# Performance work log

Hardware: AMD Instinct MI355X
Metric: run time of the kernel (lower is better)

## Reference

```python
import jax, jax.numpy as jnp
import numpy as np

D = 1024
H = 16
DH = D // H
F = 4096
B, S = 4, 2048
EPS = 1e-5


def _ln(x, g, b):
    m = jnp.mean(x, axis=-1, keepdims=True)
    v = jnp.var(x, axis=-1, keepdims=True)
    return (x - m) * jax.lax.rsqrt(v + EPS) * g + b


def setup_inputs() -> dict:
    key = jax.random.key(0)
    ks = jax.random.split(key, 16)
    s = 0.02
    return {
        "x": jax.random.normal(ks[0], (B, S, D), jnp.float32),
        "key_padding_mask": jnp.zeros((B, S), jnp.bool_),
        "Wq": jax.random.normal(ks[1], (D, D), jnp.float32) * s,
        "bq": jnp.zeros((D,), jnp.float32),
        "Wk": jax.random.normal(ks[2], (D, D), jnp.float32) * s,
        "bk": jnp.zeros((D,), jnp.float32),
        "Wv": jax.random.normal(ks[3], (D, D), jnp.float32) * s,
        "bv": jnp.zeros((D,), jnp.float32),
        "Wo": jax.random.normal(ks[4], (D, D), jnp.float32) * s,
        "bo": jnp.zeros((D,), jnp.float32),
        "W1": jax.random.normal(ks[5], (F, D), jnp.float32) * s,
        "b1": jnp.zeros((F,), jnp.float32),
        "W2": jax.random.normal(ks[6], (D, F), jnp.float32) * s,
        "b2": jnp.zeros((D,), jnp.float32),
        "ln1_g": jnp.ones((D,), jnp.float32),
        "ln1_b": jnp.zeros((D,), jnp.float32),
        "ln2_g": jnp.ones((D,), jnp.float32),
        "ln2_b": jnp.zeros((D,), jnp.float32),
    }


def _attn(x, kpm, Wq, bq, Wk, bk, Wv, bv, Wo, bo):
    b, s, d = x.shape
    scaling = DH ** (-0.5)
    q = (x @ Wq.T + bq) * scaling
    k = x @ Wk.T + bk
    v = x @ Wv.T + bv
    q = q.reshape(b, s, H, DH)
    k = k.reshape(b, s, H, DH)
    v = v.reshape(b, s, H, DH)
    # [b,h,q,k]
    scores = jnp.einsum("bqhd,bkhd->bhqk", q, k)
    scores = jnp.where(kpm[:, None, None, :], -jnp.inf, scores)
    p = jax.nn.softmax(scores.astype(jnp.float32), axis=-1).astype(q.dtype)
    out = jnp.einsum("bhqk,bkhd->bqhd", p, v).reshape(b, s, d)
    return out @ Wo.T + bo


def reference(x, key_padding_mask, Wq, bq, Wk, bk, Wv, bv, Wo, bo,
              W1, b1, W2, b2, ln1_g, ln1_b, ln2_g, ln2_b):
    # post-LN (normalize_before=False), dropout in eval mode (identity)
    x = _ln(x + _attn(x, key_padding_mask, Wq, bq, Wk, bk, Wv, bv, Wo, bo), ln1_g, ln1_b)
    h = jax.nn.gelu(x @ W1.T + b1, approximate=False)
    x = _ln(x + (h @ W2.T + b2), ln2_g, ln2_b)
    return x
```

## Files before the change

kernel.cpp:

```cpp
#include <hip/hip_runtime.h>
#include <hip/hip_bf16.h>
#include <math.h>

typedef short bf16x8 __attribute__((ext_vector_type(8)));
typedef float f32x4 __attribute__((ext_vector_type(4)));

__device__ __forceinline__ unsigned short f2bfu(float f) {
    __hip_bfloat16 h = __float2bfloat16(f);
    return __builtin_bit_cast(unsigned short, h);
}

__device__ __forceinline__ float fexp2(float x) {
    float r;
    asm("v_exp_f32 %0, %1" : "=v"(r) : "v"(x));
    return r;
}

__device__ __forceinline__ unsigned cvtpk_bf16(float lo, float hi) {
    unsigned r;
    asm("v_cvt_pk_bf16_f32 %0, %1, %2" : "=v"(r) : "v"(lo), "v"(hi));
    return r;
}

__device__ __forceinline__ float gelu_fast(float x) {
    const float x2 = x * x;
    const float z = x * (0.7978845608f + 0.0356774081f * x2);
    const float e = fexp2(z * 2.88539008f);
    const float r = __builtin_amdgcn_rcpf(e + 1.0f);
    return x * (1.0f - r);
}

__device__ __forceinline__ void gload_lds16(const void* gsrc, void* ldst) {
    __builtin_amdgcn_global_load_lds((const __attribute__((address_space(1))) void*)gsrc,
                                     (__attribute__((address_space(3))) void*)ldst,
                                     16, 0, 0);
}

__global__ __launch_bounds__(256)
void cvt_bf16_kernel(const float4* __restrict__ in, ushort4* __restrict__ out, int n4) {
    int i = blockIdx.x * 256 + threadIdx.x;
    if (i >= n4) return;
    float4 v = in[i];
    ushort4 o;
    o.x = f2bfu(v.x); o.y = f2bfu(v.y); o.z = f2bfu(v.z); o.w = f2bfu(v.w);
    out[i] = o;
}

enum { EPI_QKV = 0, EPI_RESF32 = 2, EPI_GELU = 3, EPI_RESBF16 = 5 };

template<int EPI>
__global__ __launch_bounds__(256, 3)
void gemm_bt(const __hip_bfloat16* __restrict__ A,
             const __hip_bfloat16* __restrict__ W,
             const float* __restrict__ bias,
             const void* __restrict__ resv,
             float scale,
             void* __restrict__ outp, void* __restrict__ outp2, void* __restrict__ outp3,
             int M, int N, int K)
{
    __shared__ __hip_bfloat16 As[3][128 * 32];
    __shared__ __hip_bfloat16 Ws[3][128 * 32];
    const int tid = threadIdx.x;
    const int lane = tid & 63;
    const int wid = tid >> 6;
    const int wr = wid >> 1, wc = wid & 1;
    const int g = lane >> 4, lr = lane & 15;
    const int row0 = blockIdx.x * 128;
    const int col0 = blockIdx.y * 128;

    f32x4 acc[4][4];
    const f32x4 zero = {0.f, 0.f, 0.f, 0.f};
#pragma unroll
    for (int m = 0; m < 4; ++m)
#pragma unroll
        for (int n = 0; n < 4; ++n) acc[m][n] = zero;

    const int c0 = tid, c1 = tid + 256;
    const int ar0 = c0 >> 2, ac0 = (c0 & 3) * 8;
    const int ar1 = c1 >> 2, ac1 = (c1 & 3) * 8;
    const __hip_bfloat16* Arow0 = A + (size_t)(row0 + ar0) * K + ac0;
    const __hip_bfloat16* Arow1 = A + (size_t)(row0 + ar1) * K + ac1;
    const __hip_bfloat16* Wrow0 = W + (size_t)(col0 + ar0) * K + ac0;
    const __hip_bfloat16* Wrow1 = W + (size_t)(col0 + ar1) * K + ac1;

    auto stage = [&](int bi, int k0) {
        gload_lds16(Arow0 + k0, (char*)As[bi] + c0 * 16);
        gload_lds16(Arow1 + k0, (char*)As[bi] + c1 * 16);
        gload_lds16(Wrow0 + k0, (char*)Ws[bi] + c0 * 16);
        gload_lds16(Wrow1 + k0, (char*)Ws[bi] + c1 * 16);
    };

    const int NT = K >> 5;
    stage(0, 0);
    stage(1, 32);
    asm volatile("s_waitcnt vmcnt(4)" ::: "memory");
    __builtin_amdgcn_s_barrier();
    __builtin_amdgcn_sched_barrier(0);

    int cur = 0, stg = 2;
    int kpre = 64;
    for (int t = 0; t < NT; ++t) {
        if (t + 2 < NT) stage(stg, kpre);

        bf16x8 af[4], wf[4];
#pragma unroll
        for (int m = 0; m < 4; ++m)
            af[m] = *(const bf16x8*)(As[cur] + (wr * 64 + m * 16 + lr) * 32 + g * 8);
#pragma unroll
        for (int n = 0; n < 4; ++n)
            wf[n] = *(const bf16x8*)(Ws[cur] + (wc * 64 + n * 16 + lr) * 32 + g * 8);
#pragma unroll
        for (int m = 0; m < 4; ++m)
#pragma unroll
            for (int n = 0; n < 4; ++n)
                acc[m][n] = __builtin_amdgcn_mfma_f32_16x16x32_bf16(af[m], wf[n], acc[m][n], 0, 0, 0);

        if (t + 1 < NT) {
            if (t + 2 < NT) asm volatile("s_waitcnt vmcnt(4)" ::: "memory");
            else            asm volatile("s_waitcnt vmcnt(0)" ::: "memory");
            __builtin_amdgcn_s_barrier();
            __builtin_amdgcn_sched_barrier(0);
        }
        cur = (cur == 2) ? 0 : cur + 1;
        stg = (stg == 2) ? 0 : stg + 1;
        kpre += 32;
    }

#pragma unroll
    for (int n = 0; n < 4; ++n) {
        const int cc = col0 + wc * 64 + n * 16 + lr;
        const float bv = bias[cc];
#pragma unroll
        for (int m = 0; m < 4; ++m) {
            const int rbase = row0 + wr * 64 + m * 16 + g * 4;
            if (EPI == EPI_QKV) {
                const int seg = col0 >> 10;
                if (seg == 2) {
                    ushort4 u;
                    u.x = f2bfu(acc[m][n][0] + bv);
                    u.y = f2bfu(acc[m][n][1] + bv);
                    u.z = f2bfu(acc[m][n][2] + bv);
                    u.w = f2bfu(acc[m][n][3] + bv);
                    const int cc2 = cc - 2048;
                    const int h_ = cc2 >> 6, dh = cc2 & 63;
                    const int bb = rbase >> 11;
                    const int s = rbase & 2047;
                    *(ushort4*)((__hip_bfloat16*)outp3 +
                                (((size_t)bb * 16 + h_) * 64 + dh) * 2048 + s) = u;
                } else {
                    const float sc = (seg == 0) ? scale : 1.0f;
                    __hip_bfloat16* dst = (seg == 0) ? (__hip_bfloat16*)outp
                                                     : (__hip_bfloat16*)outp2;
                    const int ccl = cc & 1023;
#pragma unroll
                    for (int r = 0; r < 4; ++r)
                        dst[(size_t)(rbase + r) * 1024 + ccl] =
                            __float2bfloat16((acc[m][n][r] + bv) * sc);
                }
            } else {
#pragma unroll
                for (int r = 0; r < 4; ++r) {
                    const size_t idx = (size_t)(rbase + r) * N + cc;
                    float v = acc[m][n][r] + bv;
                    if (EPI == EPI_RESF32) {
                        ((float*)outp)[idx] = v + ((const float*)resv)[idx];
                    } else if (EPI == EPI_RESBF16) {
                        ((float*)outp)[idx] = v +
                            __bfloat162float(((const __hip_bfloat16*)resv)[idx]);
                    } else if (EPI == EPI_GELU) {
                        ((__hip_bfloat16*)outp)[idx] = __float2bfloat16(gelu_fast(v));
                    }
                }
            }
        }
    }
}

__global__ __launch_bounds__(256, 2)
void attn_flash2(const __hip_bfloat16* __restrict__ Q,
                 const __hip_bfloat16* __restrict__ K,
                 const __hip_bfloat16* __restrict__ VT,
                 const unsigned char* __restrict__ kpm,
                 __hip_bfloat16* __restrict__ O)
{
    __shared__ __hip_bfloat16 Ks[2][64 * 64];
    __shared__ __hip_bfloat16 VTs[2][64 * 64];
    __shared__ __hip_bfloat16 Plds[4][64 * 64];

    const int tid = threadIdx.x;
    const int lane = tid & 63;
    const int w = tid >> 6;
    const int g = lane >> 4, lr = lane & 15;

    const int orig = blockIdx.y * 8 + blockIdx.x;
    const int nl = (orig & 7) * 64 + (orig >> 3);
    const int qb = nl & 7;
    const int bh = nl >> 3;

    const int b = bh >> 4, h = bh & 15;
    const int q0 = qb * 256 + w * 64;
    const size_t tokbase = (size_t)b * 2048;
    const __hip_bfloat16* VTbh = VT + (size_t)bh * 64 * 2048;

    bf16x8 qf[4][2];
#pragma unroll
    for (int qn = 0; qn < 4; ++qn)
#pragma unroll
        for (int f = 0; f < 2; ++f)
            qf[qn][f] = *(const bf16x8*)(Q + (tokbase + q0 + qn * 16 + lr) * 1024 +
                                         h * 64 + f * 32 + g * 8);

    f32x4 o[4][4];
    const f32x4 zero = {0.f, 0.f, 0.f, 0.f};
#pragma unroll
    for (int qa = 0; qa < 4; ++qa)
#pragma unroll
        for (int nd = 0; nd < 4; ++nd) o[qa][nd] = zero;
    float m_run[4], l_part[4];
#pragma unroll
    for (int qn = 0; qn < 4; ++qn) { m_run[qn] = -1e30f; l_part[qn] = 0.f; }

    __hip_bfloat16* Pw = Plds[w];
    const int rowl = lane >> 3;
    const int blkp = lane & 7;

    auto stage = [&](int bufi, int kv0) {
#pragma unroll
        for (int iss = 0; iss < 2; ++iss) {
            const int row = w * 16 + iss * 8 + rowl;
            const int sblk = blkp ^ (row & 7);
            gload_lds16(K + (tokbase + kv0 + row) * 1024 + h * 64 + sblk * 8,
                        (char*)&Ks[bufi][(w * 16 + iss * 8) * 64] + (lane & 63) * 16);
            gload_lds16(VTbh + (size_t)row * 2048 + kv0 + sblk * 8,
                        (char*)&VTs[bufi][(w * 16 + iss * 8) * 64] + (lane & 63) * 16);
        }
    };

    stage(0, 0);
    __syncthreads();
    int buf = 0;

    for (int t = 0; t < 32; ++t) {
        const int kv0 = t * 64;
        if (t < 31) stage(buf ^ 1, kv0 + 64);

        f32x4 st[4][4];
        __builtin_amdgcn_s_setprio(1);
#pragma unroll
        for (int km = 0; km < 4; ++km) {
            bf16x8 kf[2];
#pragma unroll
            for (int f = 0; f < 2; ++f)
                kf[f] = *(const bf16x8*)(&Ks[buf][(km * 16 + lr) * 64 +
                                                  (((f * 4 + g) ^ (lr & 7)) * 8)]);
#pragma unroll
            for (int qn = 0; qn < 4; ++qn) {
                st[km][qn] = __builtin_amdgcn_mfma_f32_16x16x32_bf16(kf[0], qf[qn][0], zero, 0, 0, 0);
                st[km][qn] = __builtin_amdgcn_mfma_f32_16x16x32_bf16(kf[1], qf[qn][1], st[km][qn], 0, 0, 0);
            }
        }
        __builtin_amdgcn_s_setprio(0);

        if (__any((int)(kpm[tokbase + kv0 + lane] != 0))) {
            const float NEG = -1e30f;
#pragma unroll
            for (int km = 0; km < 4; ++km) {
                const unsigned mu = *(const unsigned*)(kpm + tokbase + kv0 + km * 16 + g * 4);
#pragma unroll
                for (int r = 0; r < 4; ++r) {
                    if ((mu >> (8 * r)) & 0xFFu) {
#pragma unroll
                        for (int qn = 0; qn < 4; ++qn) st[km][qn][r] = NEG;
                    }
                }
            }
        }

        float pm[4];
#pragma unroll
        for (int qn = 0; qn < 4; ++qn) {
            float a0 = fmaxf(fmaxf(st[0][qn][0], st[0][qn][1]), fmaxf(st[0][qn][2], st[0][qn][3]));
            float a1 = fmaxf(fmaxf(st[1][qn][0], st[1][qn][1]), fmaxf(st[1][qn][2], st[1][qn][3]));
            float a2 = fmaxf(fmaxf(st[2][qn][0], st[2][qn][1]), fmaxf(st[2][qn][2], st[2][qn][3]));
            float a3 = fmaxf(fmaxf(st[3][qn][0], st[3][qn][1]), fmaxf(st[3][qn][2], st[3][qn][3]));
            pm[qn] = fmaxf(fmaxf(a0, a1), fmaxf(a2, a3));
        }
        const int trig = (pm[0] > m_run[0] + 8.f) | (pm[1] > m_run[1] + 8.f) |
                         (pm[2] > m_run[2] + 8.f) | (pm[3] > m_run[3] + 8.f);
        if (__any(trig)) {
            float alpha_q[4];
#pragma unroll
            for (int qn = 0; qn < 4; ++qn) {
                float rm = pm[qn];
                rm = fmaxf(rm, __shfl_xor(rm, 16));
                rm = fmaxf(rm, __shfl_xor(rm, 32));
                const float mnew = fmaxf(m_run[qn], rm);
                const float al = fexp2(m_run[qn] - mnew);
                l_part[qn] *= al;
                m_run[qn] = mnew;
                alpha_q[qn] = al;
            }
#pragma unroll
            for (int qa = 0; qa < 4; ++qa)
#pragma unroll
                for (int r = 0; r < 4; ++r) {
                    const float av = __shfl(alpha_q[qa], g * 4 + r, 16);
#pragma unroll
                    for (int nd = 0; nd < 4; ++nd) o[qa][nd][r] *= av;
                }
        }

#pragma unroll
        for (int qn = 0; qn < 4; ++qn) {
            const float mm = m_run[qn];
#pragma unroll
            for (int km = 0; km < 4; ++km) {
                const float p0 = fexp2(st[km][qn][0] - mm);
                const float p1 = fexp2(st[km][qn][1] - mm);
                const float p2 = fexp2(st[km][qn][2] - mm);
                const float p3 = fexp2(st[km][qn][3] - mm);
                l_part[qn] += (p0 + p1) + (p2 + p3);
                uint2 pk;
                pk.x = cvtpk_bf16(p0, p1);
                pk.y = cvtpk_bf16(p2, p3);
                const int cs = (km * 2 + (g >> 1)) ^ (lr & 7);
                *(uint2*)(Pw + (qn * 16 + lr) * 64 + cs * 8 + (g & 1) * 4) = pk;
            }
        }

        __builtin_amdgcn_s_setprio(1);
#pragma unroll
        for (int f = 0; f < 2; ++f) {
            bf16x8 pa[4];
#pragma unroll
            for (int qa = 0; qa < 4; ++qa)
                pa[qa] = *(const bf16x8*)(Pw + (qa * 16 + lr) * 64 +
                                          (((f * 4 + g) ^ (lr & 7)) * 8));
#pragma unroll
            for (int nd = 0; nd < 4; ++nd) {
                bf16x8 vb = *(const bf16x8*)(&VTs[buf][(nd * 16 + lr) * 64 +
                                                       (((f * 4 + g) ^ (lr & 7)) * 8)]);
#pragma unroll
                for (int qa = 0; qa < 4; ++qa)
                    o[qa][nd] = __builtin_amdgcn_mfma_f32_16x16x32_bf16(pa[qa], vb, o[qa][nd], 0, 0, 0);
            }
        }
        __builtin_amdgcn_s_setprio(0);

        __syncthreads();
        buf ^= 1;
    }

    float linv[4];
#pragma unroll
    for (int qn = 0; qn < 4; ++qn) {
        float lt = l_part[qn];
        lt += __shfl_xor(lt, 16);
        lt += __shfl_xor(lt, 32);
        linv[qn] = 1.0f / lt;
    }
#pragma unroll
    for (int qa = 0; qa < 4; ++qa)
#pragma unroll
        for (int r = 0; r < 4; ++r) {
            const float lv = __shfl(linv[qa], g * 4 + r, 16);
            const size_t row = tokbase + q0 + qa * 16 + g * 4 + r;
#pragma unroll
            for (int nd = 0; nd < 4; ++nd)
                O[row * 1024 + h * 64 + nd * 16 + lr] = __float2bfloat16(o[qa][nd][r] * lv);
        }
}

__global__ __launch_bounds__(256)
void ln_kernel(const float* __restrict__ in, const float* __restrict__ gamma,
               const float* __restrict__ beta, float* __restrict__ outf,
               __hip_bfloat16* __restrict__ outb)
{
    const int row = blockIdx.x;
    const int tid = threadIdx.x;
    float4 v = ((const float4*)(in + (size_t)row * 1024))[tid];
    float s = v.x + v.y + v.z + v.w;
    float s2 = v.x * v.x + v.y * v.y + v.z * v.z + v.w * v.w;
#pragma unroll
    for (int off = 1; off < 64; off <<= 1) {
        s += __shfl_xor(s, off);
        s2 += __shfl_xor(s2, off);
    }
    __shared__ float red[8];
    const int wv = tid >> 6;
    if ((tid & 63) == 0) { red[wv] = s; red[4 + wv] = s2; }
    __syncthreads();
    s = red[0] + red[1] + red[2] + red[3];
    s2 = red[4] + red[5] + red[6] + red[7];
    const float mean = s * (1.f / 1024.f);
    const float var = s2 * (1.f / 1024.f) - mean * mean;
    const float rstd = rsqrtf(var + 1e-5f);
    float4 gm = ((const float4*)gamma)[tid];
    float4 bt = ((const float4*)beta)[tid];
    float4 y;
    y.x = (v.x - mean) * rstd * gm.x + bt.x;
    y.y = (v.y - mean) * rstd * gm.y + bt.y;
    y.z = (v.z - mean) * rstd * gm.z + bt.z;
    y.w = (v.w - mean) * rstd * gm.w + bt.w;
    if (outf) ((float4*)(outf + (size_t)row * 1024))[tid] = y;
    if (outb) {
        ushort4 ub;
        ub.x = f2bfu(y.x); ub.y = f2bfu(y.y); ub.z = f2bfu(y.z); ub.w = f2bfu(y.w);
        ((ushort4*)outb)[row * 256 + tid] = ub;
    }
}

extern "C" void kernel_launch(void* const* d_in, const int* in_sizes, int n_in,
                              void* d_out, int out_size, void* d_ws, size_t ws_size,
                              hipStream_t stream)
{
    const float* x    = (const float*)d_in[0];
    const unsigned char* kpm = (const unsigned char*)d_in[1];
    const float* Wq = (const float*)d_in[2];
    const float* bq = (const float*)d_in[3];
    const float* Wk = (const float*)d_in[4];
    const float* bk = (const float*)d_in[5];
    const float* Wv = (const float*)d_in[6];
    const float* bv = (const float*)d_in[7];
    const float* Wo = (const float*)d_in[8];
    const float* bo = (const float*)d_in[9];
    const float* W1 = (const float*)d_in[10];
    const float* b1 = (const float*)d_in[11];
    const float* W2 = (const float*)d_in[12];
    const float* b2 = (const float*)d_in[13];
    const float* ln1g = (const float*)d_in[14];
    const float* ln1b = (const float*)d_in[15];
    const float* ln2g = (const float*)d_in[16];
    const float* ln2b = (const float*)d_in[17];
    float* out = (float*)d_out;

    char* ws = (char*)d_ws;
    const size_t SZ_ND2 = (size_t)8192 * 1024 * 2;
    size_t off = 0;
    __hip_bfloat16* xb  = (__hip_bfloat16*)(ws + off); off += SZ_ND2;
    __hip_bfloat16* wqb = (__hip_bfloat16*)(ws + off); off += (size_t)1024 * 1024 * 2;
    __hip_bfloat16* wkb = (__hip_bfloat16*)(ws + off); off += (size_t)1024 * 1024 * 2;
    __hip_bfloat16* wvb = (__hip_bfloat16*)(ws + off); off += (size_t)1024 * 1024 * 2;
    __hip_bfloat16* wob = (__hip_bfloat16*)(ws + off); off += (size_t)1024 * 1024 * 2;
    __hip_bfloat16* w1b = (__hip_bfloat16*)(ws + off); off += (size_t)4096 * 1024 * 2;
    __hip_bfloat16* w2b = (__hip_bfloat16*)(ws + off); off += (size_t)4096 * 1024 * 2;
    const size_t qkv0 = off;
    __hip_bfloat16* qbp = (__hip_bfloat16*)(ws + off); off += SZ_ND2;
    __hip_bfloat16* kbp = (__hip_bfloat16*)(ws + off); off += SZ_ND2;
    __hip_bfloat16* vtg = (__hip_bfloat16*)(ws + off); off += SZ_ND2;
    __hip_bfloat16* abp = (__hip_bfloat16*)(ws + off); off += SZ_ND2;
    __hip_bfloat16* hbp = (__hip_bfloat16*)(ws + qkv0);
    float* y1 = (float*)(ws + off); off += (size_t)8192 * 1024 * 4;
    __hip_bfloat16* x1b = (__hip_bfloat16*)(ws + off); off += SZ_ND2;
    float* y2 = y1;

    float* bqkv = (float*)(ws + off); off += 3072 * 4;

    auto cvt = [&](const float* src, void* dst, int n) {
        cvt_bf16_kernel<<<n / 1024, 256, 0, stream>>>((const float4*)src, (ushort4*)dst, n / 4);
    };
    cvt(x,  xb,  8192 * 1024);
    cvt(Wq, wqb, 1024 * 1024);
    cvt(Wk, wkb, 1024 * 1024);
    cvt(Wv, wvb, 1024 * 1024);
    cvt(Wo, wob, 1024 * 1024);
    cvt(W1, w1b, 4096 * 1024);
    cvt(W2, w2b, 4096 * 1024);
    hipMemcpyAsync(bqkv,        bq, 4096, hipMemcpyDeviceToDevice, stream);
    hipMemcpyAsync(bqkv + 1024, bk, 4096, hipMemcpyDeviceToDevice, stream);
    hipMemcpyAsync(bqkv + 2048, bv, 4096, hipMemcpyDeviceToDevice, stream);

    dim3 blk(256);

    const float qscale = 0.125f * 1.44269504088896f;
    gemm_bt<EPI_QKV><<<dim3(64, 24), blk, 0, stream>>>(
        xb, wqb, bqkv, nullptr, qscale, qbp, kbp, vtg, 8192, 3072, 1024);

    attn_flash2<<<dim3(8, 64), blk, 0, stream>>>(qbp, kbp, vtg, kpm, abp);

    gemm_bt<EPI_RESF32><<<dim3(64, 8), blk, 0, stream>>>(
        abp, wob, bo, x, 1.0f, y1, nullptr, nullptr, 8192, 1024, 1024);
    ln_kernel<<<8192, 256, 0, stream>>>(y1, ln1g, ln1b, nullptr, x1b);

    gemm_bt<EPI_GELU><<<dim3(64, 32), blk, 0, stream>>>(
        x1b, w1b, b1, nullptr, 1.0f, hbp, nullptr, nullptr, 8192, 4096, 1024);
    gemm_bt<EPI_RESBF16><<<dim3(64, 8), blk, 0, stream>>>(
        hbp, w2b, b2, x1b, 1.0f, y2, nullptr, nullptr, 8192, 1024, 4096);
    ln_kernel<<<8192, 256, 0, stream>>>(y2, ln2g, ln2b, out, nullptr);
}
```

Baseline: 437.0 us.

## Single-buffer K/V in attention with split staging and raise occupancy to 3

The attention kernel drops the double-buffered K and V LDS tiles for single buffers. K for the next tile is now loaded after the QK^T MFMAs and V after the PV MFMAs, each behind its own barrier, with explicit vmcnt waits. This frees LDS so launch bounds can rise to 3 blocks per CU. The key padding mask is also precomputed once per block into a per-tile bitmask instead of being checked with a per-iteration wave vote. The cost is less prefetch distance and extra barriers per iteration, traded against higher occupancy.

```diff
diff --git a/kernel.cpp b/kernel.cpp
--- a/kernel.cpp
+++ b/kernel.cpp
@@ -35,6 +35,8 @@
                                      (__attribute__((address_space(3))) void*)ldst,
                                      16, 0, 0);
 }
+
+#define MFMA __builtin_amdgcn_mfma_f32_16x16x32_bf16
 
 __global__ __launch_bounds__(256)
 void cvt_bf16_kernel(const float4* __restrict__ in, ushort4* __restrict__ out, int n4) {
@@ -113,7 +115,7 @@
         for (int m = 0; m < 4; ++m)
 #pragma unroll
             for (int n = 0; n < 4; ++n)
-                acc[m][n] = __builtin_amdgcn_mfma_f32_16x16x32_bf16(af[m], wf[n], acc[m][n], 0, 0, 0);
+                acc[m][n] = MFMA(af[m], wf[n], acc[m][n], 0, 0, 0);
 
         if (t + 1 < NT) {
             if (t + 2 < NT) asm volatile("s_waitcnt vmcnt(4)" ::: "memory");
@@ -176,15 +178,15 @@
     }
 }
 
-__global__ __launch_bounds__(256, 2)
-void attn_flash2(const __hip_bfloat16* __restrict__ Q,
+__global__ __launch_bounds__(256, 3)
+void attn_flash3(const __hip_bfloat16* __restrict__ Q,
                  const __hip_bfloat16* __restrict__ K,
                  const __hip_bfloat16* __restrict__ VT,
                  const unsigned char* __restrict__ kpm,
                  __hip_bfloat16* __restrict__ O)
 {
-    __shared__ __hip_bfloat16 Ks[2][64 * 64];
-    __shared__ __hip_bfloat16 VTs[2][64 * 64];
+    __shared__ __hip_bfloat16 Ks[64 * 64];
+    __shared__ __hip_bfloat16 VTs[64 * 64];
     __shared__ __hip_bfloat16 Plds[4][64 * 64];
 
     const int tid = threadIdx.x;
@@ -202,6 +204,16 @@
     const size_t tokbase = (size_t)b * 2048;
     const __hip_bfloat16* VTbh = VT + (size_t)bh * 64 * 2048;
 
+    unsigned tmask = 0;
+#pragma unroll
+    for (int i = 0; i < 8; ++i) {
+        const unsigned mv = *(const unsigned*)(kpm + tokbase + i * 256 + lane * 4);
+        const unsigned long long bal = __ballot((int)(mv != 0u));
+#pragma unroll
+        for (int j = 0; j < 4; ++j)
+            if ((bal >> (16 * j)) & 0xFFFFull) tmask |= (1u << (i * 4 + j));
+    }
+
     bf16x8 qf[4][2];
 #pragma unroll
     for (int qn = 0; qn < 4; ++qn)
@@ -224,25 +236,32 @@
     const int rowl = lane >> 3;
     const int blkp = lane & 7;
 
-    auto stage = [&](int bufi, int kv0) {
+    auto stageK = [&](int kv0) {
 #pragma unroll
         for (int iss = 0; iss < 2; ++iss) {
             const int row = w * 16 + iss * 8 + rowl;
             const int sblk = blkp ^ (row & 7);
             gload_lds16(K + (tokbase + kv0 + row) * 1024 + h * 64 + sblk * 8,
-                        (char*)&Ks[bufi][(w * 16 + iss * 8) * 64] + (lane & 63) * 16);
+                        (char*)&Ks[(w * 16 + iss * 8) * 64] + lane * 16);
+        }
+    };
+    auto stageV = [&](int kv0) {
+#pragma unroll
+        for (int iss = 0; iss < 2; ++iss) {
+            const int row = w * 16 + iss * 8 + rowl;
+            const int sblk = blkp ^ (row & 7);
             gload_lds16(VTbh + (size_t)row * 2048 + kv0 + sblk * 8,
-                        (char*)&VTs[bufi][(w * 16 + iss * 8) * 64] + (lane & 63) * 16);
+                        (char*)&VTs[(w * 16 + iss * 8) * 64] + lane * 16);
         }
     };
 
-    stage(0, 0);
-    __syncthreads();
-    int buf = 0;
+    stageK(0);
+    stageV(0);
+    asm volatile("s_waitcnt vmcnt(0)" ::: "memory");
+    __builtin_amdgcn_s_barrier();
 
     for (int t = 0; t < 32; ++t) {
         const int kv0 = t * 64;
-        if (t < 31) stage(buf ^ 1, kv0 + 64);
 
         f32x4 st[4][4];
         __builtin_amdgcn_s_setprio(1);
@@ -251,17 +270,19 @@
             bf16x8 kf[2];
 #pragma unroll
             for (int f = 0; f < 2; ++f)
-                kf[f] = *(const bf16x8*)(&Ks[buf][(km * 16 + lr) * 64 +
-                                                  (((f * 4 + g) ^ (lr & 7)) * 8)]);
+                kf[f] = *(const bf16x8*)(&Ks[(km * 16 + lr) * 64 +
+                                             (((f * 4 + g) ^ (lr & 7)) * 8)]);
 #pragma unroll
             for (int qn = 0; qn < 4; ++qn) {
-                st[km][qn] = __builtin_amdgcn_mfma_f32_16x16x32_bf16(kf[0], qf[qn][0], zero, 0, 0, 0);
-                st[km][qn] = __builtin_amdgcn_mfma_f32_16x16x32_bf16(kf[1], qf[qn][1], st[km][qn], 0, 0, 0);
+                st[km][qn] = MFMA(kf[0], qf[qn][0], zero, 0, 0, 0);
+                st[km][qn] = MFMA(kf[1], qf[qn][1], st[km][qn], 0, 0, 0);
             }
         }
         __builtin_amdgcn_s_setprio(0);
-
-        if (__any((int)(kpm[tokbase + kv0 + lane] != 0))) {
+        __builtin_amdgcn_s_barrier();
+        if (t < 31) stageK(kv0 + 64);
+
+        if (tmask & (1u << t)) {
             const float NEG = -1e30f;
 #pragma unroll
             for (int km = 0; km < 4; ++km) {
@@ -328,6 +349,9 @@
             }
         }
 
+        if (t == 31) asm volatile("s_waitcnt vmcnt(0)" ::: "memory");
+        else         asm volatile("s_waitcnt vmcnt(2)" ::: "memory");
+
         __builtin_amdgcn_s_setprio(1);
 #pragma unroll
         for (int f = 0; f < 2; ++f) {
@@ -338,17 +362,19 @@
                                           (((f * 4 + g) ^ (lr & 7)) * 8));
 #pragma unroll
             for (int nd = 0; nd < 4; ++nd) {
-                bf16x8 vb = *(const bf16x8*)(&VTs[buf][(nd * 16 + lr) * 64 +
-                                                       (((f * 4 + g) ^ (lr & 7)) * 8)]);
+                bf16x8 vb = *(const bf16x8*)(&VTs[(nd * 16 + lr) * 64 +
+                                                  (((f * 4 + g) ^ (lr & 7)) * 8)]);
 #pragma unroll
                 for (int qa = 0; qa < 4; ++qa)
-                    o[qa][nd] = __builtin_amdgcn_mfma_f32_16x16x32_bf16(pa[qa], vb, o[qa][nd], 0, 0, 0);
+                    o[qa][nd] = MFMA(pa[qa], vb, o[qa][nd], 0, 0, 0);
             }
         }
         __builtin_amdgcn_s_setprio(0);
-
-        __syncthreads();
-        buf ^= 1;
+        __builtin_amdgcn_s_barrier();
+        if (t < 31) {
+            stageV(kv0 + 64);
+            asm volatile("s_waitcnt vmcnt(2)" ::: "memory");
+        }
     }
 
     float linv[4];
@@ -453,7 +479,6 @@
     float* y1 = (float*)(ws + off); off += (size_t)8192 * 1024 * 4;
     __hip_bfloat16* x1b = (__hip_bfloat16*)(ws + off); off += SZ_ND2;
     float* y2 = y1;
-
     float* bqkv = (float*)(ws + off); off += 3072 * 4;
 
     auto cvt = [&](const float* src, void* dst, int n) {
@@ -471,12 +496,12 @@
     hipMemcpyAsync(bqkv + 2048, bv, 4096, hipMemcpyDeviceToDevice, stream);
 
     dim3 blk(256);
-
     const float qscale = 0.125f * 1.44269504088896f;
+
     gemm_bt<EPI_QKV><<<dim3(64, 24), blk, 0, stream>>>(
         xb, wqb, bqkv, nullptr, qscale, qbp, kbp, vtg, 8192, 3072, 1024);
 
-    attn_flash2<<<dim3(8, 64), blk, 0, stream>>>(qbp, kbp, vtg, kpm, abp);
+    attn_flash3<<<dim3(8, 64), blk, 0, stream>>>(qbp, kbp, vtg, kpm, abp);
 
     gemm_bt<EPI_RESF32><<<dim3(64, 8), blk, 0, stream>>>(
         abp, wob, bo, x, 1.0f, y1, nullptr, nullptr, 8192, 1024, 1024);
```

After: 605.2 us. +38.5%, slower.
